# Kernel optimization log

Measured on AMD Instinct MI355X. Metric: run time of the kernel, lower is better.

## Reference

```python
import jax, jax.numpy as jnp
import numpy as np

B, S, D, H = 2, 2048, 2048, 16
HD = D // H          # head_dim = 128
FF = 8192            # intermediate_size
LN_EPS = 1e-05
BIT_EPS = 1e-05


def _rope_tables(seq_len, head_dim):
    inv_freq = 1.0 / (10000.0 ** (np.arange(0, head_dim, 2, dtype=np.float64) / head_dim))
    ang = np.arange(seq_len, dtype=np.float64)[:, None] * inv_freq[None, :]  # [S, HD/2]
    ang = np.concatenate([ang, ang], axis=-1)  # [S, HD]
    return jnp.asarray(np.cos(ang), jnp.float32), jnp.asarray(np.sin(ang), jnp.float32)


def setup_inputs() -> dict:
    key = jax.random.key(0)
    ks = jax.random.split(key, 9)
    hidden_states = jax.random.normal(ks[0], (B, S, D), jnp.float32)
    # causal additive mask [1, S, S]
    causal = jnp.tril(jnp.ones((S, S), bool))
    attention_mask = jnp.where(causal, 0.0, -1e9)[None].astype(jnp.float32)
    cos, sin = _rope_tables(S, HD)
    w = lambda k, o, i: jax.random.normal(k, (o, i), jnp.float32) * 0.02
    return {
        'hidden_states': hidden_states,
        'attention_mask': attention_mask,
        'cos': cos, 'sin': sin,
        'wq': w(ks[1], D, D), 'wk': w(ks[2], D, D),
        'wv': w(ks[3], D, D), 'wo': w(ks[4], D, D),
        'wg': w(ks[5], FF, D), 'wu': w(ks[6], FF, D), 'wd': w(ks[7], D, FF),
        'ln1_w': jnp.ones((D,), jnp.float32),
        'ln2_w': jnp.ones((D,), jnp.float32),
    }


def bitlinear(x, w):
    # ternarize: clamp(round(w / (mean|w| + eps)), -1, 1); int8 cast in torch
    # breaks grad through the ternary values -> stop_gradient here.
    scale = jnp.mean(jnp.abs(w))
    tern = jax.lax.stop_gradient(jnp.clip(jnp.round(w / (scale + BIT_EPS)), -1.0, 1.0))
    # dequant = ternary * mean|w|, then standard linear (x @ W^T)
    return jnp.einsum('bsi,oi->bso', x, tern * scale)


def rmsnorm(x, w, eps=LN_EPS):
    var = jnp.mean(jnp.square(x.astype(jnp.float32)), axis=-1, keepdims=True)
    return w * (x * jax.lax.rsqrt(var + eps))


def rotate_half(x):
    x1, x2 = jnp.split(x, 2, axis=-1)
    return jnp.concatenate([-x2, x1], axis=-1)


def apply_rope(q, k, cos, sin):
    # q, k: [B, S, D] -> per-head rope -> back to [B, S, D]
    qh = q.reshape(B, S, H, HD)
    kh = k.reshape(B, S, H, HD)
    c = cos[None, :, None, :]
    s = sin[None, :, None, :]
    qe = qh * c + rotate_half(qh) * s
    ke = kh * c + rotate_half(kh) * s
    return qe.reshape(B, S, D), ke.reshape(B, S, D)


def reference(hidden_states, attention_mask, cos, sin,
              wq, wk, wv, wo, wg, wu, wd, ln1_w, ln2_w):
    residual = hidden_states
    # --- attention block ---
    x = rmsnorm(hidden_states, ln1_w)
    q = bitlinear(x, wq)
    k = bitlinear(x, wk)
    v = bitlinear(x, wv)
    q, k = apply_rope(q, k, cos, sin)
    # NOTE: scores over FULL hidden dim (no head split), scaled by sqrt(head_dim),
    # exactly as in the original module.
    scores = jnp.einsum('bsd,btd->bst', q, k) / jnp.sqrt(jnp.float32(HD))
    scores = scores + attention_mask
    probs = jax.nn.softmax(scores, axis=-1)
    attn_out = jnp.einsum('bst,btd->bsd', probs, v)
    attn_out = bitlinear(attn_out, wo)
    h = residual + attn_out
    # --- MLP block ---
    residual = h
    y = rmsnorm(h, ln2_w)
    gated = bitlinear(y, wg) * bitlinear(y, wu)
    out = bitlinear(gated, wd)
    return residual + out
```

## Files before the change

kernel.cpp:

```cpp
#include <hip/hip_runtime.h>
#include <stdint.h>

#define DEV __device__ __forceinline__

typedef __attribute__((ext_vector_type(8))) short short8;
typedef __attribute__((ext_vector_type(8))) __bf16 bf16x8;
typedef __attribute__((ext_vector_type(4))) float f32x4;

DEV unsigned short f2bf(float f) {
  union { float f; unsigned int u; } v; v.f = f;
  unsigned int r = v.u + 0x7fffu + ((v.u >> 16) & 1u);
  return (unsigned short)(r >> 16);
}
DEV float bf2f(unsigned short h) {
  union { unsigned int u; float f; } v; v.u = ((unsigned int)h) << 16;
  return v.f;
}
DEV f32x4 mfma16(short8 a, short8 b, f32x4 c) {
  return __builtin_amdgcn_mfma_f32_16x16x32_bf16(
      __builtin_bit_cast(bf16x8, a), __builtin_bit_cast(bf16x8, b), c, 0, 0, 0);
}
DEV void gload_lds16(const void* g, void* lds) {
  __builtin_amdgcn_global_load_lds(
      (const __attribute__((address_space(1))) void*)g,
      (__attribute__((address_space(3))) void*)lds, 16, 0, 0);
}

struct MArgs {
  const float* src[7];
  unsigned short* dst[7];
  int n[7];
  int sidx[7];
};

__global__ __launch_bounds__(256) void absmean_partial_multi(
    MArgs a, float* __restrict__ partial) {
  const int m = blockIdx.y;
  const float4* w4 = (const float4*)a.src[m];
  const int n4 = a.n[m] >> 2;
  float s = 0.f;
  for (int i = blockIdx.x * 256 + threadIdx.x; i < n4; i += 1024 * 256) {
    float4 v = w4[i];
    s += fabsf(v.x) + fabsf(v.y) + fabsf(v.z) + fabsf(v.w);
  }
#pragma unroll
  for (int mm = 1; mm < 64; mm <<= 1) s += __shfl_xor(s, mm);
  __shared__ float red[4];
  if ((threadIdx.x & 63) == 0) red[threadIdx.x >> 6] = s;
  __syncthreads();
  if (threadIdx.x == 0)
    partial[m * 1024 + blockIdx.x] = red[0] + red[1] + red[2] + red[3];
}

__global__ __launch_bounds__(256) void absmean_final(
    const float* __restrict__ partial, float* __restrict__ scales) {
  __shared__ double red[256];
  const int m = blockIdx.x;
  double s = 0.0;
  for (int i = threadIdx.x; i < 1024; i += 256) s += (double)partial[m * 1024 + i];
  red[threadIdx.x] = s;
  __syncthreads();
  for (int t = 128; t > 0; t >>= 1) {
    if (threadIdx.x < t) red[threadIdx.x] += red[threadIdx.x + t];
    __syncthreads();
  }
  if (threadIdx.x == 0) {
    const long long cnt = (m < 4) ? 4194304ll : 16777216ll;
    scales[m] = (float)(red[0] / (double)cnt);
  }
}

__global__ __launch_bounds__(256) void quantize_multi(
    MArgs a, const float* __restrict__ scales) {
  const int m = blockIdx.y;
  const float sc = scales[a.sidx[m]];
  const float inv = 1.f / (sc + 1e-5f);
  const float4* src = (const float4*)a.src[m];
  ushort4* dst = (ushort4*)a.dst[m];
  const int n4 = a.n[m] >> 2;
  for (int i = blockIdx.x * 256 + threadIdx.x; i < n4; i += 2048 * 256) {
    float4 v = src[i];
    ushort4 o;
    o.x = f2bf(fminf(fmaxf(rintf(v.x * inv), -1.f), 1.f) * sc);
    o.y = f2bf(fminf(fmaxf(rintf(v.y * inv), -1.f), 1.f) * sc);
    o.z = f2bf(fminf(fmaxf(rintf(v.z * inv), -1.f), 1.f) * sc);
    o.w = f2bf(fminf(fmaxf(rintf(v.w * inv), -1.f), 1.f) * sc);
    dst[i] = o;
  }
}

__global__ __launch_bounds__(256) void rmsnorm_k(
    const float* __restrict__ x, const float* __restrict__ wt,
    unsigned short* __restrict__ out) {
  const long long t = blockIdx.x;
  const float* xr = x + t * 2048;
  const int i0 = threadIdx.x * 8;
  float4 a = *(const float4*)(xr + i0);
  float4 b = *(const float4*)(xr + i0 + 4);
  float ss = a.x * a.x + a.y * a.y + a.z * a.z + a.w * a.w +
             b.x * b.x + b.y * b.y + b.z * b.z + b.w * b.w;
#pragma unroll
  for (int m = 1; m < 64; m <<= 1) ss += __shfl_xor(ss, m);
  __shared__ float red[4];
  if ((threadIdx.x & 63) == 0) red[threadIdx.x >> 6] = ss;
  __syncthreads();
  float tot = red[0] + red[1] + red[2] + red[3];
  float rs = rsqrtf(tot * (1.f / 2048.f) + 1e-5f);
  float4 wa = *(const float4*)(wt + i0);
  float4 wb = *(const float4*)(wt + i0 + 4);
  ushort4 o1, o2;
  o1.x = f2bf(a.x * wa.x * rs); o1.y = f2bf(a.y * wa.y * rs);
  o1.z = f2bf(a.z * wa.z * rs); o1.w = f2bf(a.w * wa.w * rs);
  o2.x = f2bf(b.x * wb.x * rs); o2.y = f2bf(b.y * wb.y * rs);
  o2.z = f2bf(b.z * wb.z * rs); o2.w = f2bf(b.w * wb.w * rs);
  *(ushort4*)(out + t * 2048 + i0) = o1;
  *(ushort4*)(out + t * 2048 + i0 + 4) = o2;
}

__global__ __launch_bounds__(256) void rope_k(
    const unsigned short* __restrict__ qkv, const float* __restrict__ cosT,
    const float* __restrict__ sinT, unsigned short* __restrict__ qr,
    unsigned short* __restrict__ kr, unsigned short* __restrict__ vt) {
  const long long gid = (long long)blockIdx.x * 256 + threadIdx.x;
  const int t = (int)(gid >> 10);
  const int r = (int)(gid & 1023);
  const int h = r >> 6, d = r & 63;
  const int s = t & 2047, b = t >> 11;
  const unsigned short* row = qkv + (long long)t * 6144;
  const float c = cosT[s * 128 + d], sn = sinT[s * 128 + d];
  const int col = h * 128 + d;
  const float SC = 0.08838834764831845f;
  float q1 = bf2f(row[col]), q2 = bf2f(row[col + 64]);
  float k1 = bf2f(row[2048 + col]), k2 = bf2f(row[2048 + col + 64]);
  long long ob = (long long)t * 2048 + col;
  qr[ob] = f2bf((q1 * c - q2 * sn) * SC);
  qr[ob + 64] = f2bf((q2 * c + q1 * sn) * SC);
  kr[ob] = f2bf(k1 * c - k2 * sn);
  kr[ob + 64] = f2bf(k2 * c + k1 * sn);
  vt[((long long)b * 2048 + col) * 2048 + s] = row[4096 + col];
  vt[((long long)b * 2048 + col + 64) * 2048 + s] = row[4096 + col + 64];
}

__global__ __launch_bounds__(256) void softmax_causal(
    const float* __restrict__ scores, unsigned short* __restrict__ probs) {
  const int r = blockIdx.x;
  const int s = r & 2047;
  const float* src = scores + (long long)r * 2048;
  unsigned short* dst = probs + (long long)r * 2048;
  const int L = s + 1;
  __shared__ float red[4];
  float mx = -1e30f;
  for (int j = threadIdx.x; j < L; j += 256) mx = fmaxf(mx, src[j]);
#pragma unroll
  for (int m = 1; m < 64; m <<= 1) mx = fmaxf(mx, __shfl_xor(mx, m));
  if ((threadIdx.x & 63) == 0) red[threadIdx.x >> 6] = mx;
  __syncthreads();
  mx = fmaxf(fmaxf(red[0], red[1]), fmaxf(red[2], red[3]));
  float sum = 0.f;
  for (int j = threadIdx.x; j < L; j += 256) sum += __expf(src[j] - mx);
  __syncthreads();
#pragma unroll
  for (int m = 1; m < 64; m <<= 1) sum += __shfl_xor(sum, m);
  if ((threadIdx.x & 63) == 0) red[threadIdx.x >> 6] = sum;
  __syncthreads();
  const float inv = 1.f / (red[0] + red[1] + red[2] + red[3]);
  for (int j = threadIdx.x; j < 2048; j += 256)
    dst[j] = (j < L) ? f2bf(__expf(src[j] - mx) * inv) : (unsigned short)0;
}

template <int EPI, int CAUSAL>
__global__ __launch_bounds__(256) void gemm_nt(
    const unsigned short* __restrict__ A, const unsigned short* __restrict__ Bw,
    void* __restrict__ Cp, int M, int N, int K,
    long long sAz, long long sBz, long long sCz) {
  const long long m0 = (long long)blockIdx.y * 128;
  const long long n0 = (long long)blockIdx.x * 128;
  if (CAUSAL == 1 && n0 > m0 + 127) return;
  __shared__ __align__(16) unsigned short sA[2][128 * 32];
  __shared__ __align__(16) unsigned short sB[2][128 * 32];
  const int tid = threadIdx.x;
  const int w = tid >> 6, l = tid & 63;
  const long long z = blockIdx.z;
  A += z * sAz;
  Bw += z * sBz;
  const long long cofs = z * sCz;
  const int wr = w >> 1, wc = w & 1;
  const int lrow = l & 15, lk = (l >> 4) * 8;

  f32x4 acc[4][4] = {};
  int nk = K >> 5;
  if (CAUSAL == 2) nk = (int)((m0 + 128) >> 5);
  int cur = 0;

  auto stage = [&](int buf, int k0) {
#pragma unroll
    for (int i = 0; i < 2; ++i) {
      const int flat = (w * 2 + i) * 64 + l;
      const int row = flat >> 2;
      const int col = (flat & 3) * 8;
      gload_lds16(&A[(m0 + row) * K + k0 + col], (char*)&sA[buf][0] + (w * 2 + i) * 1024);
      gload_lds16(&Bw[(n0 + row) * K + k0 + col], (char*)&sB[buf][0] + (w * 2 + i) * 1024);
    }
  };

  stage(0, 0);
  __syncthreads();
  for (int kt = 0; kt < nk; ++kt) {
    if (kt + 1 < nk) stage(cur ^ 1, (kt + 1) << 5);
    short8 af[4], bfr[4];
#pragma unroll
    for (int m = 0; m < 4; ++m)
      af[m] = *(const short8*)&sA[cur][(wr * 64 + m * 16 + lrow) * 32 + lk];
#pragma unroll
    for (int n = 0; n < 4; ++n)
      bfr[n] = *(const short8*)&sB[cur][(wc * 64 + n * 16 + lrow) * 32 + lk];
#pragma unroll
    for (int m = 0; m < 4; ++m)
#pragma unroll
      for (int n = 0; n < 4; ++n)
        acc[m][n] = mfma16(af[m], bfr[n], acc[m][n]);
    __syncthreads();
    cur ^= 1;
  }

  const int orow = (l >> 4) * 4, ocol = l & 15;
#pragma unroll
  for (int m = 0; m < 4; ++m)
#pragma unroll
    for (int n = 0; n < 4; ++n)
#pragma unroll
      for (int r = 0; r < 4; ++r) {
        long long gr = m0 + wr * 64 + m * 16 + orow + r;
        long long gc = n0 + wc * 64 + n * 16 + ocol;
        long long idx = cofs + gr * N + gc;
        float v = acc[m][n][r];
        if (EPI == 0) ((unsigned short*)Cp)[idx] = f2bf(v);
        else ((float*)Cp)[idx] = v;
      }
}

template <int EPI>
__global__ __launch_bounds__(512, 2) void gemm256(
    const unsigned short* __restrict__ A, const unsigned short* __restrict__ Bw,
    void* __restrict__ Cp, const void* __restrict__ Ep,
    int N, int K, int nbx, int kLen, int nChunks, long long zCout) {
  __shared__ __align__(16) unsigned short lds[4 * 2 * 8192];
  __shared__ __align__(16) unsigned short ldsDummy[512];
  const int tid = threadIdx.x;
  const int wid = tid >> 6, l = tid & 63;
  const int wr = wid >> 2, wcn = wid & 3;

  const int nwg = gridDim.x;
  const int q8 = nwg >> 3;
  const int lin = (blockIdx.x & 7) * q8 + (blockIdx.x >> 3);
  const int t32 = lin >> 5, r32 = lin & 31;
  const int tpr = nbx >> 3;
  const int tm = t32 / tpr, tn = t32 - tm * tpr;
  const long long m0 = (long long)(tm * 4 + (r32 >> 3)) * 256;
  const long long n0 = (long long)(tn * 8 + (r32 & 7)) * 256;
  const int z = blockIdx.z;
  const long long kbase = (long long)z * kLen;
  const long long zofs = (long long)z * zCout;

  const int stRow = (l >> 2);
  const int stCol = (((l & 3) ^ ((l >> 3) & 3))) * 8;
  auto stage = [&](int chunk, int mat) {
    char* base = (char*)lds + (((chunk & 3) * 2 + mat) * 16384);
    const unsigned short* src = mat ? Bw : A;
    const long long rb = mat ? n0 : m0;
    if (chunk < nChunks) {
      const long long kcol = kbase + (long long)chunk * 32 + stCol;
#pragma unroll
      for (int i = 0; i < 2; ++i) {
        const int row = (wid * 2 + i) * 16 + stRow;
        gload_lds16(&src[(rb + row) * K + kcol], base + (wid * 2 + i) * 1024);
      }
    } else {
#pragma unroll
      for (int i = 0; i < 2; ++i) gload_lds16(&src[rb * K], (char*)ldsDummy);
    }
  };

  const int ar = l & 15;
  const int rj = ((l >> 4) ^ ((l >> 1) & 3)) << 4;

  f32x4 acc[8][4] = {};

  stage(0, 0); stage(0, 1);
  stage(1, 0); stage(1, 1);
  stage(2, 0); stage(2, 1);
  asm volatile("s_waitcnt vmcnt(8)" ::: "memory");
  __builtin_amdgcn_s_barrier();

  for (int c = 0; c < nChunks; ++c) {
    const int slot = c & 3;
    const char* sA = (const char*)lds + (slot * 2 + 0) * 16384;
    const char* sB = (const char*)lds + (slot * 2 + 1) * 16384;
    short8 af[4], bf[4];
#pragma unroll
    for (int m = 0; m < 4; ++m)
      af[m] = *(const short8*)(sA + (wr * 128 + m * 16 + ar) * 64 + rj);
#pragma unroll
    for (int n = 0; n < 4; ++n)
      bf[n] = *(const short8*)(sB + (wcn * 64 + n * 16 + ar) * 64 + rj);
    stage(c + 3, 0);
    __builtin_amdgcn_s_barrier();
    asm volatile("s_waitcnt lgkmcnt(0)" ::: "memory");
    __builtin_amdgcn_sched_barrier(0);
    __builtin_amdgcn_s_setprio(1);
#pragma unroll
    for (int m = 0; m < 4; ++m)
#pragma unroll
      for (int n = 0; n < 4; ++n) acc[m][n] = mfma16(af[m], bf[n], acc[m][n]);
    __builtin_amdgcn_s_setprio(0);
    __builtin_amdgcn_s_barrier();
#pragma unroll
    for (int m = 0; m < 4; ++m)
      af[m] = *(const short8*)(sA + (wr * 128 + (m + 4) * 16 + ar) * 64 + rj);
    stage(c + 3, 1);
    __builtin_amdgcn_s_barrier();
    asm volatile("s_waitcnt lgkmcnt(0)" ::: "memory");
    __builtin_amdgcn_sched_barrier(0);
    __builtin_amdgcn_s_setprio(1);
#pragma unroll
    for (int m = 0; m < 4; ++m)
#pragma unroll
      for (int n = 0; n < 4; ++n)
        acc[m + 4][n] = mfma16(af[m], bf[n], acc[m + 4][n]);
    __builtin_amdgcn_s_setprio(0);
    asm volatile("s_waitcnt vmcnt(8)" ::: "memory");
    __builtin_amdgcn_s_barrier();
  }
  asm volatile("s_waitcnt vmcnt(0)" ::: "memory");
  __builtin_amdgcn_s_barrier();

  const int orow = (l >> 4) * 4, ocol = l & 15;
#pragma unroll
  for (int m = 0; m < 8; ++m)
#pragma unroll
    for (int n = 0; n < 4; ++n)
#pragma unroll
      for (int r = 0; r < 4; ++r) {
        const long long gr = m0 + wr * 128 + m * 16 + orow + r;
        const long long gc = n0 + wcn * 64 + n * 16 + ocol;
        const long long idx = zofs + gr * N + gc;
        const float v = acc[m][n][r];
        if (EPI == 0) {
          ((unsigned short*)Cp)[idx] = f2bf(v);
        } else if (EPI == 2) {
          ((unsigned short*)Cp)[idx] = f2bf(bf2f(((const unsigned short*)Ep)[idx]) * v);
        } else {
          ((float*)Cp)[idx] = v;
        }
      }
}

__global__ __launch_bounds__(256) void combine2(
    const float* __restrict__ ep, const float* __restrict__ p,
    float* __restrict__ out, long long n4) {
  const float4* e4 = (const float4*)ep;
  const float4* p4 = (const float4*)p;
  float4* o4 = (float4*)out;
  for (long long i = blockIdx.x * 256 + threadIdx.x; i < n4; i += 2048 * 256) {
    float4 a = e4[i], b = p4[i], c = p4[i + n4];
    float4 o;
    o.x = a.x + b.x + c.x; o.y = a.y + b.y + c.y;
    o.z = a.z + b.z + c.z; o.w = a.w + b.w + c.w;
    o4[i] = o;
  }
}

extern "C" void kernel_launch(void* const* d_in, const int* in_sizes, int n_in,
                              void* d_out, int out_size, void* d_ws, size_t ws_size,
                              hipStream_t stream) {
  (void)in_sizes; (void)n_in; (void)out_size; (void)ws_size;
  const float* hidden = (const float*)d_in[0];
  const float* cosT = (const float*)d_in[2];
  const float* sinT = (const float*)d_in[3];
  const float* wq = (const float*)d_in[4];
  const float* wk = (const float*)d_in[5];
  const float* wv = (const float*)d_in[6];
  const float* wo = (const float*)d_in[7];
  const float* wg = (const float*)d_in[8];
  const float* wu = (const float*)d_in[9];
  const float* wd = (const float*)d_in[10];
  const float* ln1 = (const float*)d_in[11];
  const float* ln2 = (const float*)d_in[12];

  const size_t MB = 1ull << 20;
  char* ws = (char*)d_ws;
  unsigned short* xn    = (unsigned short*)(ws + 0);
  unsigned short* wqkvq = (unsigned short*)(ws + 16 * MB);
  unsigned short* qkv   = (unsigned short*)(ws + 40 * MB);
  unsigned short* qrb   = (unsigned short*)(ws + 88 * MB);
  unsigned short* krb   = (unsigned short*)(ws + 104 * MB);
  unsigned short* vtb   = (unsigned short*)(ws + 120 * MB);
  float*          scoresB = (float*)(ws + 0);
  unsigned short* probsB  = (unsigned short*)(ws + 40 * MB);
  float*          part   = (float*)(ws + 0);
  unsigned short* wgq   = (unsigned short*)(ws + 0);
  unsigned short* wuq   = (unsigned short*)(ws + 32 * MB);
  unsigned short* gbuf  = (unsigned short*)(ws + 64 * MB);
  unsigned short* attnb = (unsigned short*)(ws + 136 * MB);
  unsigned short* woq   = (unsigned short*)(ws + 152 * MB);
  float*          hbuf  = (float*)(ws + 160 * MB);
  unsigned short* ybuf  = (unsigned short*)(ws + 192 * MB);
  unsigned short* gated = (unsigned short*)(ws + 208 * MB);
  unsigned short* wdq   = (unsigned short*)(ws + 272 * MB);
  float* wspart         = (float*)(ws + 304 * MB);
  float* scales         = (float*)(ws + 304 * MB + 32768);

  MArgs am;
  am.src[0] = wq; am.src[1] = wk; am.src[2] = wv; am.src[3] = wo;
  am.src[4] = wg; am.src[5] = wu; am.src[6] = wd;
  am.n[0] = am.n[1] = am.n[2] = am.n[3] = 4194304;
  am.n[4] = am.n[5] = am.n[6] = 16777216;
  for (int i = 0; i < 7; ++i) { am.dst[i] = nullptr; am.sidx[i] = i; }
  absmean_partial_multi<<<dim3(1024, 7), 256, 0, stream>>>(am, wspart);
  absmean_final<<<7, 256, 0, stream>>>(wspart, scales);

  MArgs qe;
  qe.src[0] = wq; qe.dst[0] = wqkvq;            qe.n[0] = 4194304;  qe.sidx[0] = 0;
  qe.src[1] = wk; qe.dst[1] = wqkvq + 4194304;  qe.n[1] = 4194304;  qe.sidx[1] = 1;
  qe.src[2] = wv; qe.dst[2] = wqkvq + 8388608;  qe.n[2] = 4194304;  qe.sidx[2] = 2;
  qe.src[3] = wo; qe.dst[3] = woq;              qe.n[3] = 4194304;  qe.sidx[3] = 3;
  qe.src[4] = wd; qe.dst[4] = wdq;              qe.n[4] = 16777216; qe.sidx[4] = 6;
  qe.src[5] = wq; qe.dst[5] = nullptr; qe.n[5] = 0; qe.sidx[5] = 0;
  qe.src[6] = wq; qe.dst[6] = nullptr; qe.n[6] = 0; qe.sidx[6] = 0;
  quantize_multi<<<dim3(2048, 5), 256, 0, stream>>>(qe, scales);

  rmsnorm_k<<<4096, 256, 0, stream>>>(hidden, ln1, xn);

  gemm256<0><<<dim3(384, 1, 1), 512, 0, stream>>>(
      xn, wqkvq, qkv, nullptr, 6144, 2048, 24, 2048, 64, 0);

  rope_k<<<16384, 256, 0, stream>>>(qkv, cosT, sinT, qrb, krb, vtb);

  gemm_nt<4, 1><<<dim3(16, 16, 2), 256, 0, stream>>>(
      qrb, krb, scoresB, 2048, 2048, 2048, 4194304, 4194304, 4194304);
  softmax_causal<<<4096, 256, 0, stream>>>(scoresB, probsB);
  gemm_nt<0, 2><<<dim3(16, 16, 2), 256, 0, stream>>>(
      probsB, vtb, attnb, 2048, 2048, 2048, 4194304, 4194304, 4194304);

  gemm256<4><<<dim3(128, 1, 2), 512, 0, stream>>>(
      attnb, woq, part, nullptr, 2048, 2048, 8, 1024, 32, 8388608);
  combine2<<<2048, 256, 0, stream>>>(hidden, part, hbuf, 2097152);

  MArgs ql;
  ql.src[0] = wg; ql.dst[0] = wgq; ql.n[0] = 16777216; ql.sidx[0] = 4;
  ql.src[1] = wu; ql.dst[1] = wuq; ql.n[1] = 16777216; ql.sidx[1] = 5;
  for (int i = 2; i < 7; ++i) { ql.src[i] = wg; ql.dst[i] = nullptr; ql.n[i] = 0; ql.sidx[i] = 0; }
  quantize_multi<<<dim3(2048, 2), 256, 0, stream>>>(ql, scales);

  rmsnorm_k<<<4096, 256, 0, stream>>>(hbuf, ln2, ybuf);

  gemm256<0><<<dim3(512, 1, 1), 512, 0, stream>>>(
      ybuf, wgq, gbuf, nullptr, 8192, 2048, 32, 2048, 64, 0);
  gemm256<2><<<dim3(512, 1, 1), 512, 0, stream>>>(
      ybuf, wuq, gated, gbuf, 8192, 2048, 32, 2048, 64, 0);

  gemm256<4><<<dim3(128, 1, 2), 512, 0, stream>>>(
      gated, wdq, part, nullptr, 2048, 8192, 8, 4096, 128, 8388608);
  combine2<<<2048, 256, 0, stream>>>(hbuf, part, (float*)d_out, 2097152);
}
```

Baseline: 880.0 us.

## Switch gemm256 to 32x32x16 MFMA with 64-wide K stages and double buffering

The 256x256 GEMM kernel now uses 32x32x16 bf16 MFMA instructions instead of 16x16x32, with larger 64-element K chunks staged into a two-slot LDS buffer (was four slots of 32). The LDS swizzle, fragment loads and epilogue index mapping are rewritten for the 32x32 output layout. Launch arguments are halved to count the new 64-wide K groups. The goal is fewer LDS reads per FLOP and fewer barriers per K. In exchange, prefetch depth drops to one stage ahead and the stage is issued after the compute, which may expose memory latency.

Result: slower. 982.5 us (+11.6%).

```diff
diff --git a/kernel.cpp b/kernel.cpp
--- a/kernel.cpp
+++ b/kernel.cpp
@@ -6,6 +6,7 @@
 typedef __attribute__((ext_vector_type(8))) short short8;
 typedef __attribute__((ext_vector_type(8))) __bf16 bf16x8;
 typedef __attribute__((ext_vector_type(4))) float f32x4;
+typedef __attribute__((ext_vector_type(16))) float f32x16;
 
 DEV unsigned short f2bf(float f) {
   union { float f; unsigned int u; } v; v.f = f;
@@ -18,6 +19,10 @@
 }
 DEV f32x4 mfma16(short8 a, short8 b, f32x4 c) {
   return __builtin_amdgcn_mfma_f32_16x16x32_bf16(
+      __builtin_bit_cast(bf16x8, a), __builtin_bit_cast(bf16x8, b), c, 0, 0, 0);
+}
+DEV f32x16 mfma32(short8 a, short8 b, f32x16 c) {
+  return __builtin_amdgcn_mfma_f32_32x32x16_bf16(
       __builtin_bit_cast(bf16x8, a), __builtin_bit_cast(bf16x8, b), c, 0, 0, 0);
 }
 DEV void gload_lds16(const void* g, void* lds) {
@@ -243,8 +248,8 @@
 __global__ __launch_bounds__(512, 2) void gemm256(
     const unsigned short* __restrict__ A, const unsigned short* __restrict__ Bw,
     void* __restrict__ Cp, const void* __restrict__ Ep,
-    int N, int K, int nbx, int kLen, int nChunks, long long zCout) {
-  __shared__ __align__(16) unsigned short lds[4 * 2 * 8192];
+    int N, int K, int nbx, int kLen, int ng, long long zCout) {
+  __shared__ __align__(16) unsigned short lds[2 * 2 * 16384];
   __shared__ __align__(16) unsigned short ldsDummy[512];
   const int tid = threadIdx.x;
   const int wid = tid >> 6, l = tid & 63;
@@ -262,87 +267,107 @@
   const long long kbase = (long long)z * kLen;
   const long long zofs = (long long)z * zCout;
 
-  const int stRow = (l >> 2);
-  const int stCol = (((l & 3) ^ ((l >> 3) & 3))) * 8;
-  auto stage = [&](int chunk, int mat) {
-    char* base = (char*)lds + (((chunk & 3) * 2 + mat) * 16384);
-    const unsigned short* src = mat ? Bw : A;
-    const long long rb = mat ? n0 : m0;
-    if (chunk < nChunks) {
-      const long long kcol = kbase + (long long)chunk * 32 + stCol;
-#pragma unroll
-      for (int i = 0; i < 2; ++i) {
-        const int row = (wid * 2 + i) * 16 + stRow;
-        gload_lds16(&src[(rb + row) * K + kcol], base + (wid * 2 + i) * 1024);
+  const int sRow = l >> 3;
+  const int sCol = ((l & 7) ^ (l >> 3)) * 8;
+  auto stage = [&](int g) {
+    if (g < ng) {
+      const long long kcol = kbase + (long long)g * 64 + sCol;
+      char* base = (char*)lds + (g & 1) * 65536;
+#pragma unroll
+      for (int mat = 0; mat < 2; ++mat) {
+        const unsigned short* src = mat ? Bw : A;
+        const long long rb = mat ? n0 : m0;
+#pragma unroll
+        for (int li = 0; li < 4; ++li) {
+          const int r = wid * 32 + li * 8 + sRow;
+          gload_lds16(&src[(rb + r) * K + kcol],
+                      base + mat * 32768 + (wid * 4 + li) * 1024);
+        }
       }
     } else {
 #pragma unroll
-      for (int i = 0; i < 2; ++i) gload_lds16(&src[rb * K], (char*)ldsDummy);
+      for (int i = 0; i < 8; ++i) gload_lds16(&A[m0 * K], (char*)ldsDummy);
     }
   };
 
-  const int ar = l & 15;
-  const int rj = ((l >> 4) ^ ((l >> 1) & 3)) << 4;
-
-  f32x4 acc[8][4] = {};
-
-  stage(0, 0); stage(0, 1);
-  stage(1, 0); stage(1, 1);
-  stage(2, 0); stage(2, 1);
+  const int rl31 = l & 31, rl7 = l & 7, rhi = l >> 5;
+
+  f32x16 acc[4][2] = {};
+
+  stage(0);
+  stage(1);
   asm volatile("s_waitcnt vmcnt(8)" ::: "memory");
   __builtin_amdgcn_s_barrier();
 
-  for (int c = 0; c < nChunks; ++c) {
-    const int slot = c & 3;
-    const char* sA = (const char*)lds + (slot * 2 + 0) * 16384;
-    const char* sB = (const char*)lds + (slot * 2 + 1) * 16384;
-    short8 af[4], bf[4];
-#pragma unroll
-    for (int m = 0; m < 4; ++m)
-      af[m] = *(const short8*)(sA + (wr * 128 + m * 16 + ar) * 64 + rj);
-#pragma unroll
-    for (int n = 0; n < 4; ++n)
-      bf[n] = *(const short8*)(sB + (wcn * 64 + n * 16 + ar) * 64 + rj);
-    stage(c + 3, 0);
+  for (int g = 0; g < ng; ++g) {
+    const char* sA = (const char*)lds + (g & 1) * 65536;
+    const char* sB = sA + 32768;
+    short8 af[2][4], bf[2][4];
+#pragma unroll
+    for (int m = 0; m < 2; ++m)
+#pragma unroll
+      for (int s = 0; s < 4; ++s) {
+        const int row = wr * 128 + m * 32 + rl31;
+        const int w = (s * 2 + rhi) ^ rl7;
+        af[m][s] = *(const short8*)(sA + row * 128 + w * 16);
+      }
+#pragma unroll
+    for (int n = 0; n < 2; ++n)
+#pragma unroll
+      for (int s = 0; s < 4; ++s) {
+        const int row = wcn * 64 + n * 32 + rl31;
+        const int w = (s * 2 + rhi) ^ rl7;
+        bf[n][s] = *(const short8*)(sB + row * 128 + w * 16);
+      }
     __builtin_amdgcn_s_barrier();
     asm volatile("s_waitcnt lgkmcnt(0)" ::: "memory");
     __builtin_amdgcn_sched_barrier(0);
     __builtin_amdgcn_s_setprio(1);
 #pragma unroll
-    for (int m = 0; m < 4; ++m)
-#pragma unroll
-      for (int n = 0; n < 4; ++n) acc[m][n] = mfma16(af[m], bf[n], acc[m][n]);
+    for (int m = 0; m < 2; ++m)
+#pragma unroll
+      for (int n = 0; n < 2; ++n)
+#pragma unroll
+        for (int s = 0; s < 4; ++s)
+          acc[m][n] = mfma32(af[m][s], bf[n][s], acc[m][n]);
     __builtin_amdgcn_s_setprio(0);
     __builtin_amdgcn_s_barrier();
 #pragma unroll
-    for (int m = 0; m < 4; ++m)
-      af[m] = *(const short8*)(sA + (wr * 128 + (m + 4) * 16 + ar) * 64 + rj);
-    stage(c + 3, 1);
+    for (int m = 0; m < 2; ++m)
+#pragma unroll
+      for (int s = 0; s < 4; ++s) {
+        const int row = wr * 128 + (m + 2) * 32 + rl31;
+        const int w = (s * 2 + rhi) ^ rl7;
+        af[m][s] = *(const short8*)(sA + row * 128 + w * 16);
+      }
     __builtin_amdgcn_s_barrier();
     asm volatile("s_waitcnt lgkmcnt(0)" ::: "memory");
     __builtin_amdgcn_sched_barrier(0);
     __builtin_amdgcn_s_setprio(1);
 #pragma unroll
-    for (int m = 0; m < 4; ++m)
-#pragma unroll
-      for (int n = 0; n < 4; ++n)
-        acc[m + 4][n] = mfma16(af[m], bf[n], acc[m + 4][n]);
+    for (int m = 0; m < 2; ++m)
+#pragma unroll
+      for (int n = 0; n < 2; ++n)
+#pragma unroll
+        for (int s = 0; s < 4; ++s)
+          acc[m + 2][n] = mfma32(af[m][s], bf[n][s], acc[m + 2][n]);
     __builtin_amdgcn_s_setprio(0);
+    __builtin_amdgcn_s_barrier();
+    stage(g + 2);
     asm volatile("s_waitcnt vmcnt(8)" ::: "memory");
     __builtin_amdgcn_s_barrier();
   }
-  asm volatile("s_waitcnt vmcnt(0)" ::: "memory");
-  __builtin_amdgcn_s_barrier();
-
-  const int orow = (l >> 4) * 4, ocol = l & 15;
-#pragma unroll
-  for (int m = 0; m < 8; ++m)
-#pragma unroll
-    for (int n = 0; n < 4; ++n)
-#pragma unroll
-      for (int r = 0; r < 4; ++r) {
-        const long long gr = m0 + wr * 128 + m * 16 + orow + r;
-        const long long gc = n0 + wcn * 64 + n * 16 + ocol;
+
+  const long long cm = m0 + wr * 128;
+  const long long cn = n0 + wcn * 64;
+#pragma unroll
+  for (int m = 0; m < 4; ++m)
+#pragma unroll
+    for (int n = 0; n < 2; ++n)
+#pragma unroll
+      for (int r = 0; r < 16; ++r) {
+        const long long gr = cm + m * 32 + (r & 3) + 8 * (r >> 2) + 4 * rhi;
+        const long long gc = cn + n * 32 + rl31;
         const long long idx = zofs + gr * N + gc;
         const float v = acc[m][n][r];
         if (EPI == 0) {
@@ -432,7 +457,7 @@
   rmsnorm_k<<<4096, 256, 0, stream>>>(hidden, ln1, xn);
 
   gemm256<0><<<dim3(384, 1, 1), 512, 0, stream>>>(
-      xn, wqkvq, qkv, nullptr, 6144, 2048, 24, 2048, 64, 0);
+      xn, wqkvq, qkv, nullptr, 6144, 2048, 24, 2048, 32, 0);
 
   rope_k<<<16384, 256, 0, stream>>>(qkv, cosT, sinT, qrb, krb, vtb);
 
@@ -443,7 +468,7 @@
       probsB, vtb, attnb, 2048, 2048, 2048, 4194304, 4194304, 4194304);
 
   gemm256<4><<<dim3(128, 1, 2), 512, 0, stream>>>(
-      attnb, woq, part, nullptr, 2048, 2048, 8, 1024, 32, 8388608);
+      attnb, woq, part, nullptr, 2048, 2048, 8, 1024, 16, 8388608);
   combine2<<<2048, 256, 0, stream>>>(hidden, part, hbuf, 2097152);
 
   MArgs ql;
@@ -455,11 +480,11 @@
   rmsnorm_k<<<4096, 256, 0, stream>>>(hbuf, ln2, ybuf);
 
   gemm256<0><<<dim3(512, 1, 1), 512, 0, stream>>>(
-      ybuf, wgq, gbuf, nullptr, 8192, 2048, 32, 2048, 64, 0);
+      ybuf, wgq, gbuf, nullptr, 8192, 2048, 32, 2048, 32, 0);
   gemm256<2><<<dim3(512, 1, 1), 512, 0, stream>>>(
-      ybuf, wuq, gated, gbuf, 8192, 2048, 32, 2048, 64, 0);
+      ybuf, wuq, gated, gbuf, 8192, 2048, 32, 2048, 32, 0);
 
   gemm256<4><<<dim3(128, 1, 2), 512, 0, stream>>>(
-      gated, wdq, part, nullptr, 2048, 8192, 8, 4096, 128, 8388608);
+      gated, wdq, part, nullptr, 2048, 8192, 8, 4096, 64, 8388608);
   combine2<<<2048, 256, 0, stream>>>(hbuf, part, (float*)d_out, 2097152);
 }
```
